# Optimization experiments

Hardware: AMD Instinct MI355X
Metric: run time of the kernel (lower is better)

## Reference

```python
import jax, jax.numpy as jnp
import numpy as np

B, D, S = 128, 256, 512
K, H, NCLS = 50, 256, 2
THRES = 0.3  # conceptshap threshold


def _l2norm(x, axis):
    n = jnp.sqrt(jnp.sum(x * x, axis=axis, keepdims=True))
    return x / jnp.maximum(n, 1e-12)


def setup_inputs() -> dict:
    key = jax.random.key(0)
    ks = jax.random.split(key, 6)
    return {
        "f_input": jax.random.normal(ks[0], (B, D, S), dtype=jnp.float32),
        "targets": jax.random.uniform(ks[1], (B,), dtype=jnp.float32),
        "topic_vector": jax.random.uniform(ks[2], (D, K), minval=-0.5, maxval=0.5, dtype=jnp.float32),
        "rec_vector_1": jax.random.uniform(ks[3], (K, H), minval=-0.5, maxval=0.5, dtype=jnp.float32),
        "rec_vector_2": jax.random.uniform(ks[4], (H, D), minval=-0.5, maxval=0.5, dtype=jnp.float32),
        "Wc": jax.random.normal(ks[5], (D, NCLS), dtype=jnp.float32) * 0.05,
        "bc": jnp.zeros((NCLS,), dtype=jnp.float32),
        "causal": 0,
    }


def reference(f_input, targets, topic_vector, rec_vector_1, rec_vector_2, Wc, bc, causal):
    # text path (n=3), model_name != 'transformer' -> swap to [B, S, D]
    x = jnp.swapaxes(f_input, 1, 2)                # [B, S, D]
    x_n = _l2norm(x, axis=-1)                      # F.normalize(dim=n-1)
    tv_n = _l2norm(topic_vector, axis=0)           # [D, K], column-normalized

    topic_prob = jnp.einsum('bsd,dk->bsk', x, tv_n)      # [B, S, K]
    topic_prob_n = jnp.einsum('bsd,dk->bsk', x_n, tv_n)  # [B, S, K]

    # conceptshap: no softmax, hard threshold mask
    mask = (topic_prob_n > THRES).astype(topic_prob.dtype)
    topic_prob_am = topic_prob * mask
    topic_prob_sum = jnp.sum(topic_prob_am, axis=-1, keepdims=True) + 0.001
    topic_prob_nn = topic_prob_am / (topic_prob_sum + 1e-8)

    rec_layer_1 = jax.nn.relu(jnp.einsum('bsk,kh->bsh', topic_prob_nn, rec_vector_1))
    rec_layer_2 = jnp.einsum('bsh,hd->bsd', rec_layer_1, rec_vector_2)  # [B, S, D]

    ae_loss = jnp.mean((x_n - rec_layer_2) ** 2)

    rec_out = jnp.swapaxes(rec_layer_2, 1, 2)      # back to [B, D, S]
    # frozen classifier: mean over seq + linear head
    pred = jnp.mean(rec_out, axis=-1) @ Wc + bc    # [B, NCLS]

    # concept_sim: mean of per-concept top-(B//4) similarity scores, negated
    res = topic_prob_n.reshape(-1, K).T            # [K, B*S]
    topv, _ = jax.lax.top_k(res, B // 4)
    concept_sim = -jnp.mean(topv)

    concept_far = jnp.mean(tv_n.T @ tv_n - jnp.eye(K, dtype=tv_n.dtype))

    return (pred, jnp.float32(0.0), concept_sim, concept_far, topic_prob_nn, ae_loss)
```

## Files before the change

kernel.cpp:

```cpp
#include <hip/hip_runtime.h>
#include <math.h>

#define BB 128
#define DD 256
#define SS 512
#define KK 50
#define HH 256
#define TS 64
#define NBLK (BB * SS / TS)
#define BS (BB * SS)

#define CHUNK 1024
#define NCH (BS / CHUNK)
#define NCHBLK (KK * NCH / 4)
#define TOPK 32
#define MAXSURV 512
#define NSUB (TS / 16)

#define TVN_OFF 0
#define TVNT_OFF (TVN_OFF + DD * KK)
#define TPNT_OFF (TVNT_OFF + KK * DD)
#define PREDACC_OFF (TPNT_OFF + KK * BS)
#define AE_OFF (PREDACC_OFF + BB * DD)
#define SIM_OFF (AE_OFF + 1)
#define CNT_OFF (AE_OFF + 2)
#define SIMD_OFF (AE_OFF + 3)
#define LIST_OFF (AE_OFF + 4)
#define CAND_OFF (LIST_OFF + MAXSURV)
#define NZERO (BB * DD + 4)

#define OUT_NN_OFF 259
#define OUT_AE_IDX (OUT_NN_OFF + KK * BS)

__device__ __forceinline__ unsigned fkey(float f) {
  unsigned u = __float_as_uint(f);
  return (u & 0x80000000u) ? ~u : (u | 0x80000000u);
}
__device__ __forceinline__ float keyval(unsigned T) {
  unsigned u = (T & 0x80000000u) ? (T & 0x7FFFFFFFu) : ~T;
  return __uint_as_float(u);
}

__global__ __launch_bounds__(256) void tvn_kernel(const float* __restrict__ tv,
                                                  float* __restrict__ tvn,
                                                  float* __restrict__ tvnT,
                                                  float* __restrict__ zbase) {
  __shared__ float red[256];
  const int k = blockIdx.x, t = threadIdx.x;
  {
    const int gid = k * 256 + t;
    for (int i = gid; i < NZERO; i += KK * 256) zbase[i] = 0.0f;
  }
  float v = tv[t * KK + k];
  red[t] = v * v;
  __syncthreads();
  for (int off = 128; off > 0; off >>= 1) {
    if (t < off) red[t] += red[t + off];
    __syncthreads();
  }
  float inv = 1.0f / fmaxf(sqrtf(red[0]), 1e-12f);
  const float nv = v * inv;
  tvn[t * KK + k] = nv;
  tvnT[k * DD + t] = nv;
}

__global__ __launch_bounds__(256, 4) void main_kernel(
    const float* __restrict__ f_input, const float* __restrict__ tvnT,
    float* __restrict__ out_nn, float* __restrict__ tpn_t,
    float* __restrict__ ae_acc, int* __restrict__ surv_cnt,
    int* __restrict__ surv_list) {
  __shared__ int wflag[4];

  const int blk = blockIdx.x;
  const int b = blk >> 3;
  const int s0 = (blk & 7) * TS;
  const int t = threadIdx.x;
  const int lane = t & 63;
  const int wid = t >> 6;
  const int kb = __builtin_amdgcn_readfirstlane(wid);

  const float* tvk[13];
  bool kval[13];
  #pragma unroll
  for (int j = 0; j < 13; ++j) {
    const int k = 4 * j + kb;
    kval[j] = (k < KK);
    tvk[j] = tvnT + (size_t)(kval[j] ? k : (KK - 1)) * DD;
  }

  const float* xp = f_input + (size_t)b * DD * SS + s0 + lane;

  float acc[13];
  #pragma unroll
  for (int j = 0; j < 13; ++j) acc[j] = 0.0f;

  float xb[2][4];
  #pragma unroll
  for (int i = 0; i < 4; ++i) xb[0][i] = xp[(size_t)i * SS];

  float s2 = 0.0f;
  int buf = 0;
  for (int part = 0; part < 8; ++part) {
    float p = 0.0f;
    #pragma unroll
    for (int dd = 0; dd < 32; dd += 4) {
      const int d0 = part * 32 + dd;
      const int dn = (d0 + 4 < DD) ? (d0 + 4) : 0;
      #pragma unroll
      for (int i = 0; i < 4; ++i) xb[buf ^ 1][i] = xp[(size_t)(dn + i) * SS];
      const float x0 = xb[buf][0], x1 = xb[buf][1], x2 = xb[buf][2], x3 = xb[buf][3];
      p += x0 * x0; p += x1 * x1; p += x2 * x2; p += x3 * x3;
      #pragma unroll
      for (int j = 0; j < 13; ++j) {
        const float4 tq = *(const float4*)(tvk[j] + d0);
        acc[j] += x0 * tq.x; acc[j] += x1 * tq.y;
        acc[j] += x2 * tq.z; acc[j] += x3 * tq.w;
      }
      buf ^= 1;
    }
    s2 = (part == 0) ? p : (s2 + p);
  }
  const float invn = 1.0f / fmaxf(sqrtf(s2), 1e-12f);

  bool m = false;
  const size_t gs = (size_t)b * SS + s0 + lane;
  #pragma unroll
  for (int j = 0; j < 13; ++j) {
    if (kval[j]) {
      const int k = 4 * j + kb;
      const float o = acc[j] * invn;
      tpn_t[(size_t)k * BS + gs] = o;
      m |= (o > 0.3f);
    }
  }

  const int w = __any((int)m);
  if (lane == 0) wflag[wid] = w;
  __syncthreads();
  const int any = wflag[0] | wflag[1] | wflag[2] | wflag[3];

  if (!any) {
    float* ob = out_nn + ((size_t)b * SS + s0) * KK;
    for (int p2 = t; p2 < TS * KK; p2 += 256) ob[p2] = 0.0f;
    if (t == 0) atomicAdd(ae_acc, (float)TS);
    return;
  }
  if (t == 0) {
    const int idx = atomicAdd(surv_cnt, 1);
    if (idx < MAXSURV) surv_list[idx] = blk;
  }
}

__global__ __launch_bounds__(256) void chunk_surv_kernel(
    const float* __restrict__ tpn_t, float* __restrict__ cand,
    const float* __restrict__ f_input, const float* __restrict__ rec1,
    const float* __restrict__ rec2, const int* __restrict__ surv_cnt,
    const int* __restrict__ surv_list, float* __restrict__ out_nn,
    float* __restrict__ predacc, float* __restrict__ ae_acc) {
  __shared__ __align__(16) float NNk[KK * 20];
  __shared__ __align__(16) float R1t[HH * 20];
  __shared__ float nprt[16][17];
  __shared__ float nrm[16], invn[16];
  __shared__ float pm[8 * DD];
  __shared__ float red4[4];

  const int t = threadIdx.x;
  const int lane = t & 63, wid = t >> 6;

  if (blockIdx.x < NCHBLK) {
    const int gchunk = blockIdx.x * 4 + wid;
    const int k = gchunk >> 6;
    const int c = gchunk & (NCH - 1);
    const float* row = tpn_t + (size_t)k * BS + c * CHUNK;

    float v[16];
    unsigned key[16];
    #pragma unroll
    for (int j = 0; j < 16; ++j) {
      v[j] = row[lane + j * 64];
      key[j] = fkey(v[j]);
    }
    unsigned T = 0;
    for (int bit = 31; bit >= 0; --bit) {
      const unsigned ct = T | (1u << bit);
      int cnt = 0;
      #pragma unroll
      for (int j = 0; j < 16; ++j) cnt += (key[j] >= ct) ? 1 : 0;
      #pragma unroll
      for (int off = 1; off < 64; off <<= 1) cnt += __shfl_xor(cnt, off);
      if (cnt >= TOPK) T = ct;
    }
    int cg = 0;
    #pragma unroll
    for (int j = 0; j < 16; ++j) cg += (key[j] > T) ? 1 : 0;
    int incl = cg;
    #pragma unroll
    for (int off = 1; off < 64; off <<= 1) {
      int y = __shfl_up(incl, off);
      if (lane >= off) incl += y;
    }
    const int excl = incl - cg;
    const int total_gt = __shfl(incl, 63);

    float* cb = cand + (size_t)gchunk * TOPK;
    int pos = excl;
    #pragma unroll
    for (int j = 0; j < 16; ++j) {
      if (key[j] > T) cb[pos++] = v[j];
    }
    if (lane < TOPK - total_gt) cb[total_gt + lane] = keyval(T);
    return;
  }

  const int bid = blockIdx.x - NCHBLK;
  int cnt = *surv_cnt;
  if (cnt > MAXSURV) cnt = MAXSURV;
  const int ntask = NSUB * cnt;

  for (int task = bid; task < ntask; task += 64) {
    const int blk = surv_list[task / NSUB];
    const int q = task % NSUB;
    const int b = blk >> 3;
    const int s0 = (blk & 7) * TS + q * 16;
    const float* fb = f_input + (size_t)b * DD * SS;
    const size_t gs0 = (size_t)b * SS + s0;

    for (int p = t; p < KK * 16; p += 256) {
      const int k = p >> 4, ss = p & 15;
      NNk[k * 20 + ss] = tpn_t[(size_t)k * BS + gs0 + ss];
    }
    {
      const int ss = t & 15, part = t >> 4;
      const float* xc = fb + (size_t)(part * 16) * SS + s0 + ss;
      float p = 0.0f;
      #pragma unroll
      for (int i = 0; i < 16; ++i) {
        const float v = xc[(size_t)i * SS];
        p += v * v;
      }
      nprt[part][ss] = p;
    }
    __syncthreads();
    if (t < 16) {
      float s2 = 0.0f;
      #pragma unroll
      for (int i = 0; i < 16; ++i) s2 += nprt[i][t];
      const float n = fmaxf(sqrtf(s2), 1e-12f);
      nrm[t] = n;
      invn[t] = 1.0f / n;
      float sm = 0.0f;
      for (int k = 0; k < KK; ++k) {
        const float tpn = NNk[k * 20 + t];
        sm += (tpn > 0.3f) ? tpn * n : 0.0f;
      }
      const float idv = 1.0f / (sm + 0.001f + 1e-8f);
      for (int k = 0; k < KK; ++k) {
        const float tpn = NNk[k * 20 + t];
        NNk[k * 20 + t] = (tpn > 0.3f) ? tpn * n * idv : 0.0f;
      }
    }
    __syncthreads();

    for (int p = t; p < 16 * KK; p += 256) {
      const int ss = p / KK, k = p - ss * KK;
      out_nn[(gs0 + ss) * KK + k] = NNk[k * 20 + ss];
    }

    {
      float a[16];
      #pragma unroll
      for (int i = 0; i < 16; ++i) a[i] = 0.0f;
      #pragma unroll 2
      for (int k = 0; k < KK; ++k) {
        const float r = rec1[k * HH + t];
        const float4* np = (const float4*)&NNk[k * 20];
        #pragma unroll
        for (int qq = 0; qq < 4; ++qq) {
          const float4 nv = np[qq];
          a[qq * 4 + 0] += nv.x * r;
          a[qq * 4 + 1] += nv.y * r;
          a[qq * 4 + 2] += nv.z * r;
          a[qq * 4 + 3] += nv.w * r;
        }
      }
      #pragma unroll
      for (int i = 0; i < 16; ++i) R1t[t * 20 + i] = fmaxf(a[i], 0.0f);
    }
    __syncthreads();

    const int tx = t & 31, ty = t >> 5;
    const int d0 = tx * 8, sb = ty * 2;
    float c2[2][8];
    #pragma unroll
    for (int i = 0; i < 2; ++i)
      #pragma unroll
      for (int j = 0; j < 8; ++j) c2[i][j] = 0.0f;
    for (int h0 = 0; h0 < HH; h0 += 8) {
      float4 B0[8], B1[8];
      #pragma unroll
      for (int u = 0; u < 8; ++u) {
        B0[u] = *(const float4*)(rec2 + (h0 + u) * DD + d0);
        B1[u] = *(const float4*)(rec2 + (h0 + u) * DD + d0 + 4);
      }
      #pragma unroll
      for (int u = 0; u < 8; ++u) {
        const float2 a01 = *(const float2*)(&R1t[(h0 + u) * 20 + sb]);
        const float bv[8] = {B0[u].x, B0[u].y, B0[u].z, B0[u].w,
                             B1[u].x, B1[u].y, B1[u].z, B1[u].w};
        #pragma unroll
        for (int j = 0; j < 8; ++j) {
          c2[0][j] += a01.x * bv[j];
          c2[1][j] += a01.y * bv[j];
        }
      }
    }
    #pragma unroll
    for (int j = 0; j < 8; ++j) pm[ty * DD + d0 + j] = c2[0][j] + c2[1][j];
    __syncthreads();
    {
      float sum = 0.0f;
      #pragma unroll
      for (int r = 0; r < 8; ++r) sum += pm[r * DD + t];
      atomicAdd(&predacc[(size_t)b * DD + t], sum);
    }
    float e = 0.0f;
    #pragma unroll
    for (int j = 0; j < 8; ++j) {
      #pragma unroll
      for (int i = 0; i < 2; ++i) {
        const float x = fb[(size_t)(d0 + j) * SS + s0 + sb + i];
        const float diff = x * invn[sb + i] - c2[i][j];
        e += diff * diff;
      }
    }
    #pragma unroll
    for (int off = 1; off < 64; off <<= 1) e += __shfl_xor(e, off);
    if (lane == 0) red4[wid] = e;
    __syncthreads();
    if (t == 0) atomicAdd(ae_acc, red4[0] + red4[1] + red4[2] + red4[3]);
    __syncthreads();
  }
}

__global__ __launch_bounds__(256) void merge_finalize_kernel(
    const float* __restrict__ cand, const float* __restrict__ predacc,
    const float* __restrict__ Wc, const float* __restrict__ bc,
    const float* __restrict__ ae_acc, float* __restrict__ sim_acc,
    unsigned* __restrict__ sim_done, const float* __restrict__ tvn,
    float* __restrict__ out) {
  __shared__ float r0[256], r1[256];
  const int blk = blockIdx.x;
  const int t = threadIdx.x;

  if (blk >= BB) {
    if (t < 64) {
      const int k = blk - BB;
      const int lane = t;
      const float* row = cand + (size_t)k * (NCH * TOPK);
      float v[32];
      unsigned key[32];
      #pragma unroll
      for (int j = 0; j < 32; ++j) {
        v[j] = row[lane + j * 64];
        key[j] = fkey(v[j]);
      }
      unsigned T = 0;
      for (int bit = 31; bit >= 0; --bit) {
        const unsigned ct = T | (1u << bit);
        int cnt = 0;
        #pragma unroll
        for (int j = 0; j < 32; ++j) cnt += (key[j] >= ct) ? 1 : 0;
        #pragma unroll
        for (int off = 1; off < 64; off <<= 1) cnt += __shfl_xor(cnt, off);
        if (cnt >= TOPK) T = ct;
      }
      float s = 0.0f;
      int cgt = 0;
      #pragma unroll
      for (int j = 0; j < 32; ++j) {
        if (key[j] > T) { s += v[j]; cgt++; }
      }
      #pragma unroll
      for (int off = 1; off < 64; off <<= 1) {
        s += __shfl_xor(s, off);
        cgt += __shfl_xor(cgt, off);
      }
      if (lane == 0) {
        atomicAdd(sim_acc, s + (float)(TOPK - cgt) * keyval(T));
        __threadfence();
        const unsigned c = atomicAdd(sim_done, 1u);
        if (c == KK - 1) {
          __threadfence();
          const float tot = atomicAdd(sim_acc, 0.0f);
          out[257] = -tot * (1.0f / (float)(KK * TOPK));
        }
      }
    }
    return;
  }

  const float s = predacc[(size_t)blk * DD + t];
  r0[t] = s * Wc[t * 2 + 0];
  r1[t] = s * Wc[t * 2 + 1];
  __syncthreads();
  for (int off = 128; off > 0; off >>= 1) {
    if (t < off) { r0[t] += r0[t + off]; r1[t] += r1[t + off]; }
    __syncthreads();
  }
  if (t == 0) {
    out[blk * 2 + 0] = r0[0] * (1.0f / (float)SS) + bc[0];
    out[blk * 2 + 1] = r1[0] * (1.0f / (float)SS) + bc[1];
    if (blk == 0) {
      out[256] = 0.0f;
      out[OUT_AE_IDX] = (*ae_acc) * (1.0f / ((float)BB * (float)SS * (float)DD));
    }
  }
  if (blk == 0) {
    __syncthreads();
    float rs = 0.0f;
    for (int k = 0; k < KK; ++k) rs += tvn[t * KK + k];
    r0[t] = rs * rs;
    __syncthreads();
    for (int off = 128; off > 0; off >>= 1) {
      if (t < off) r0[t] += r0[t + off];
      __syncthreads();
    }
    if (t == 0) out[258] = (r0[0] - (float)KK) / ((float)KK * (float)KK);
  }
}

extern "C" void kernel_launch(void* const* d_in, const int* in_sizes, int n_in,
                              void* d_out, int out_size, void* d_ws, size_t ws_size,
                              hipStream_t stream) {
  (void)in_sizes; (void)n_in; (void)out_size; (void)ws_size;
  const float* f_input = (const float*)d_in[0];
  const float* tv = (const float*)d_in[2];
  const float* rec1 = (const float*)d_in[3];
  const float* rec2 = (const float*)d_in[4];
  const float* Wc = (const float*)d_in[5];
  const float* bc = (const float*)d_in[6];

  float* out = (float*)d_out;
  float* ws = (float*)d_ws;
  float* tvn = ws + TVN_OFF;
  float* tvnT = ws + TVNT_OFF;
  float* tpn_t = ws + TPNT_OFF;
  float* predacc = ws + PREDACC_OFF;
  float* ae_acc = ws + AE_OFF;
  float* sim_acc = ws + SIM_OFF;
  int* surv_cnt = (int*)(ws + CNT_OFF);
  unsigned* sim_done = (unsigned*)(ws + SIMD_OFF);
  int* surv_list = (int*)(ws + LIST_OFF);
  float* cand = ws + CAND_OFF;

  tvn_kernel<<<KK, 256, 0, stream>>>(tv, tvn, tvnT, predacc);
  main_kernel<<<NBLK, 256, 0, stream>>>(f_input, tvnT, out + OUT_NN_OFF, tpn_t,
                                        ae_acc, surv_cnt, surv_list);
  chunk_surv_kernel<<<NCHBLK + 64, 256, 0, stream>>>(
      tpn_t, cand, f_input, rec1, rec2, surv_cnt, surv_list,
      out + OUT_NN_OFF, predacc, ae_acc);
  merge_finalize_kernel<<<BB + KK, 256, 0, stream>>>(
      cand, predacc, Wc, bc, ae_acc, sim_acc, sim_done, tvn, out);
}
```

Baseline: 231.0 us.

## Register-block two positions per thread and split concepts across block pairs

The projection kernel now uses 128-position tiles. Each thread loads two adjacent positions with float2 and accumulates both against every topic-vector load. Each tile's 50 concepts are split across two blocks, 8 waves with interleaved k, so per-thread accumulators stay small while topic-vector loads per FMA are halved. The all-zero decision is combined across the two blocks with a per-tile atomic flag and counter, and the block that finishes last records the survivor or the zero fill. The cost is that each input tile is now read by two blocks, plus some extra atomics and synchronisation.

```diff
diff --git a/kernel.cpp b/kernel.cpp
--- a/kernel.cpp
+++ b/kernel.cpp
@@ -6,8 +6,9 @@
 #define SS 512
 #define KK 50
 #define HH 256
-#define TS 64
-#define NBLK (BB * SS / TS)
+#define TS 128
+#define NTILES (BB * SS / TS)
+#define NBLK (NTILES * 2)
 #define BS (BB * SS)
 
 #define CHUNK 1024
@@ -25,9 +26,11 @@
 #define SIM_OFF (AE_OFF + 1)
 #define CNT_OFF (AE_OFF + 2)
 #define SIMD_OFF (AE_OFF + 3)
-#define LIST_OFF (AE_OFF + 4)
+#define TFLAG_OFF (AE_OFF + 4)
+#define TCNT_OFF (TFLAG_OFF + NTILES)
+#define NZERO (BB * DD + 4 + 2 * NTILES)
+#define LIST_OFF (TCNT_OFF + NTILES)
 #define CAND_OFF (LIST_OFF + MAXSURV)
-#define NZERO (BB * DD + 4)
 
 #define OUT_NN_OFF 259
 #define OUT_AE_IDX (OUT_NN_OFF + KK * BS)
@@ -68,86 +71,108 @@
     const float* __restrict__ f_input, const float* __restrict__ tvnT,
     float* __restrict__ out_nn, float* __restrict__ tpn_t,
     float* __restrict__ ae_acc, int* __restrict__ surv_cnt,
-    int* __restrict__ surv_list) {
+    int* __restrict__ surv_list, int* __restrict__ tile_flag,
+    int* __restrict__ tile_cnt) {
   __shared__ int wflag[4];
+  __shared__ int decision;
 
   const int blk = blockIdx.x;
-  const int b = blk >> 3;
-  const int s0 = (blk & 7) * TS;
+  const int tile = blk >> 1;
+  const int half = blk & 1;
+  const int b = tile >> 2;
+  const int s0 = (tile & 3) * TS;
   const int t = threadIdx.x;
   const int lane = t & 63;
   const int wid = t >> 6;
-  const int kb = __builtin_amdgcn_readfirstlane(wid);
-
-  const float* tvk[13];
-  bool kval[13];
+  const int kb = __builtin_amdgcn_readfirstlane(half * 4 + wid);
+
+  const float* tvk[7];
+  bool kval[7];
   #pragma unroll
-  for (int j = 0; j < 13; ++j) {
-    const int k = 4 * j + kb;
+  for (int j = 0; j < 7; ++j) {
+    const int k = kb + 8 * j;
     kval[j] = (k < KK);
     tvk[j] = tvnT + (size_t)(kval[j] ? k : (KK - 1)) * DD;
   }
 
-  const float* xp = f_input + (size_t)b * DD * SS + s0 + lane;
-
-  float acc[13];
+  const float* xp = f_input + (size_t)b * DD * SS + s0 + 2 * lane;
+
+  float acc0[7], acc1[7];
   #pragma unroll
-  for (int j = 0; j < 13; ++j) acc[j] = 0.0f;
-
-  float xb[2][4];
+  for (int j = 0; j < 7; ++j) { acc0[j] = 0.0f; acc1[j] = 0.0f; }
+
+  float2 xb[2][4];
   #pragma unroll
-  for (int i = 0; i < 4; ++i) xb[0][i] = xp[(size_t)i * SS];
-
-  float s2 = 0.0f;
+  for (int i = 0; i < 4; ++i) xb[0][i] = *(const float2*)(xp + (size_t)i * SS);
+
+  float s2_0 = 0.0f, s2_1 = 0.0f;
   int buf = 0;
   for (int part = 0; part < 8; ++part) {
-    float p = 0.0f;
+    float p0 = 0.0f, p1 = 0.0f;
     #pragma unroll
     for (int dd = 0; dd < 32; dd += 4) {
       const int d0 = part * 32 + dd;
       const int dn = (d0 + 4 < DD) ? (d0 + 4) : 0;
       #pragma unroll
-      for (int i = 0; i < 4; ++i) xb[buf ^ 1][i] = xp[(size_t)(dn + i) * SS];
-      const float x0 = xb[buf][0], x1 = xb[buf][1], x2 = xb[buf][2], x3 = xb[buf][3];
-      p += x0 * x0; p += x1 * x1; p += x2 * x2; p += x3 * x3;
-      #pragma unroll
-      for (int j = 0; j < 13; ++j) {
+      for (int i = 0; i < 4; ++i) xb[buf ^ 1][i] = *(const float2*)(xp + (size_t)(dn + i) * SS);
+      const float2 xa = xb[buf][0], xc2 = xb[buf][1], xc3 = xb[buf][2], xc4 = xb[buf][3];
+      p0 += xa.x * xa.x; p0 += xc2.x * xc2.x; p0 += xc3.x * xc3.x; p0 += xc4.x * xc4.x;
+      p1 += xa.y * xa.y; p1 += xc2.y * xc2.y; p1 += xc3.y * xc3.y; p1 += xc4.y * xc4.y;
+      #pragma unroll
+      for (int j = 0; j < 7; ++j) {
         const float4 tq = *(const float4*)(tvk[j] + d0);
-        acc[j] += x0 * tq.x; acc[j] += x1 * tq.y;
-        acc[j] += x2 * tq.z; acc[j] += x3 * tq.w;
+        acc0[j] += xa.x * tq.x; acc0[j] += xc2.x * tq.y;
+        acc0[j] += xc3.x * tq.z; acc0[j] += xc4.x * tq.w;
+        acc1[j] += xa.y * tq.x; acc1[j] += xc2.y * tq.y;
+        acc1[j] += xc3.y * tq.z; acc1[j] += xc4.y * tq.w;
       }
       buf ^= 1;
     }
-    s2 = (part == 0) ? p : (s2 + p);
-  }
-  const float invn = 1.0f / fmaxf(sqrtf(s2), 1e-12f);
+    s2_0 = (part == 0) ? p0 : (s2_0 + p0);
+    s2_1 = (part == 0) ? p1 : (s2_1 + p1);
+  }
+  const float i0 = 1.0f / fmaxf(sqrtf(s2_0), 1e-12f);
+  const float i1 = 1.0f / fmaxf(sqrtf(s2_1), 1e-12f);
 
   bool m = false;
-  const size_t gs = (size_t)b * SS + s0 + lane;
+  const size_t gs = (size_t)b * SS + s0 + 2 * lane;
   #pragma unroll
-  for (int j = 0; j < 13; ++j) {
+  for (int j = 0; j < 7; ++j) {
     if (kval[j]) {
-      const int k = 4 * j + kb;
-      const float o = acc[j] * invn;
-      tpn_t[(size_t)k * BS + gs] = o;
-      m |= (o > 0.3f);
+      const int k = kb + 8 * j;
+      float2 o;
+      o.x = acc0[j] * i0;
+      o.y = acc1[j] * i1;
+      *(float2*)(tpn_t + (size_t)k * BS + gs) = o;
+      m = m | (o.x > 0.3f) | (o.y > 0.3f);
     }
   }
 
   const int w = __any((int)m);
   if (lane == 0) wflag[wid] = w;
   __syncthreads();
-  const int any = wflag[0] | wflag[1] | wflag[2] | wflag[3];
-
-  if (!any) {
+  const int blockAny = wflag[0] | wflag[1] | wflag[2] | wflag[3];
+
+  if (t == 0) {
+    const int old = atomicOr(&tile_flag[tile], blockAny);
+    const int done = atomicAdd(&tile_cnt[tile], 1);
+    int dec = 0;
+    if (done == 1) {
+      const int fl = old | blockAny;
+      if (fl) {
+        const int idx = atomicAdd(surv_cnt, 1);
+        if (idx < MAXSURV) surv_list[idx] = tile;
+      } else {
+        atomicAdd(ae_acc, (float)TS);
+        dec = 1;
+      }
+    }
+    decision = dec;
+  }
+  __syncthreads();
+  if (decision) {
     float* ob = out_nn + ((size_t)b * SS + s0) * KK;
     for (int p2 = t; p2 < TS * KK; p2 += 256) ob[p2] = 0.0f;
-    if (t == 0) atomicAdd(ae_acc, (float)TS);
-    return;
-  }
-  if (t == 0) {
-    const int idx = atomicAdd(surv_cnt, 1);
-    if (idx < MAXSURV) surv_list[idx] = blk;
   }
 }
 
@@ -218,10 +243,10 @@
   const int ntask = NSUB * cnt;
 
   for (int task = bid; task < ntask; task += 64) {
-    const int blk = surv_list[task / NSUB];
+    const int tile = surv_list[task / NSUB];
     const int q = task % NSUB;
-    const int b = blk >> 3;
-    const int s0 = (blk & 7) * TS + q * 16;
+    const int b = tile >> 2;
+    const int s0 = (tile & 3) * TS + q * 16;
     const float* fb = f_input + (size_t)b * DD * SS;
     const size_t gs0 = (size_t)b * SS + s0;
 
@@ -450,12 +475,15 @@
   float* sim_acc = ws + SIM_OFF;
   int* surv_cnt = (int*)(ws + CNT_OFF);
   unsigned* sim_done = (unsigned*)(ws + SIMD_OFF);
+  int* tile_flag = (int*)(ws + TFLAG_OFF);
+  int* tile_cnt = (int*)(ws + TCNT_OFF);
   int* surv_list = (int*)(ws + LIST_OFF);
   float* cand = ws + CAND_OFF;
 
   tvn_kernel<<<KK, 256, 0, stream>>>(tv, tvn, tvnT, predacc);
   main_kernel<<<NBLK, 256, 0, stream>>>(f_input, tvnT, out + OUT_NN_OFF, tpn_t,
-                                        ae_acc, surv_cnt, surv_list);
+                                        ae_acc, surv_cnt, surv_list,
+                                        tile_flag, tile_cnt);
   chunk_surv_kernel<<<NCHBLK + 64, 256, 0, stream>>>(
       tpn_t, cand, f_input, rec1, rec2, surv_cnt, surv_list,
       out + OUT_NN_OFF, predacc, ae_acc);
```

Measured after the change: 226.4 us. 1.02x faster.

## Process two sequence positions per thread, prefetch rec weights, batch rec1 loads

Applied to the files above, without the earlier changes.

The main kernel tile grows from 64 to 128 positions, and each thread now computes two adjacent positions using float2 loads. This reuses each topic-vector load across twice the work and halves the block count. The surviving-tile path gets an early exit, a warm-up pass that reads rec1/rec2 into cache and writes their sum to a sink buffer, and rec1 loads batched ten at a time. The risks are higher register pressure in main_kernel (two accumulators per concept) and coarser survival granularity: one position above threshold now sends a whole 128-position tile through the slow path.

```diff
diff --git a/kernel.cpp b/kernel.cpp
--- a/kernel.cpp
+++ b/kernel.cpp
@@ -6,7 +6,7 @@
 #define SS 512
 #define KK 50
 #define HH 256
-#define TS 64
+#define TS 128
 #define NBLK (BB * SS / TS)
 #define BS (BB * SS)
 
@@ -25,9 +25,10 @@
 #define SIM_OFF (AE_OFF + 1)
 #define CNT_OFF (AE_OFF + 2)
 #define SIMD_OFF (AE_OFF + 3)
+#define NZERO (BB * DD + 4)
 #define LIST_OFF (AE_OFF + 4)
-#define CAND_OFF (LIST_OFF + MAXSURV)
-#define NZERO (BB * DD + 4)
+#define SINK_OFF (LIST_OFF + MAXSURV)
+#define CAND_OFF (SINK_OFF + 64 * 256)
 
 #define OUT_NN_OFF 259
 #define OUT_AE_IDX (OUT_NN_OFF + KK * BS)
@@ -72,8 +73,8 @@
   __shared__ int wflag[4];
 
   const int blk = blockIdx.x;
-  const int b = blk >> 3;
-  const int s0 = (blk & 7) * TS;
+  const int b = blk >> 2;
+  const int s0 = (blk & 3) * TS;
   const int t = threadIdx.x;
   const int lane = t & 63;
   const int wid = t >> 6;
@@ -88,49 +89,56 @@
     tvk[j] = tvnT + (size_t)(kval[j] ? k : (KK - 1)) * DD;
   }
 
-  const float* xp = f_input + (size_t)b * DD * SS + s0 + lane;
-
-  float acc[13];
+  const float* xp = f_input + (size_t)b * DD * SS + s0 + 2 * lane;
+
+  float acc0[13], acc1[13];
   #pragma unroll
-  for (int j = 0; j < 13; ++j) acc[j] = 0.0f;
-
-  float xb[2][4];
+  for (int j = 0; j < 13; ++j) { acc0[j] = 0.0f; acc1[j] = 0.0f; }
+
+  float2 xb[2][4];
   #pragma unroll
-  for (int i = 0; i < 4; ++i) xb[0][i] = xp[(size_t)i * SS];
-
-  float s2 = 0.0f;
+  for (int i = 0; i < 4; ++i) xb[0][i] = *(const float2*)(xp + (size_t)i * SS);
+
+  float s2_0 = 0.0f, s2_1 = 0.0f;
   int buf = 0;
   for (int part = 0; part < 8; ++part) {
-    float p = 0.0f;
+    float p0 = 0.0f, p1 = 0.0f;
     #pragma unroll
     for (int dd = 0; dd < 32; dd += 4) {
       const int d0 = part * 32 + dd;
       const int dn = (d0 + 4 < DD) ? (d0 + 4) : 0;
       #pragma unroll
-      for (int i = 0; i < 4; ++i) xb[buf ^ 1][i] = xp[(size_t)(dn + i) * SS];
-      const float x0 = xb[buf][0], x1 = xb[buf][1], x2 = xb[buf][2], x3 = xb[buf][3];
-      p += x0 * x0; p += x1 * x1; p += x2 * x2; p += x3 * x3;
+      for (int i = 0; i < 4; ++i) xb[buf ^ 1][i] = *(const float2*)(xp + (size_t)(dn + i) * SS);
+      const float2 xa = xb[buf][0], xc2 = xb[buf][1], xc3 = xb[buf][2], xc4 = xb[buf][3];
+      p0 += xa.x * xa.x; p0 += xc2.x * xc2.x; p0 += xc3.x * xc3.x; p0 += xc4.x * xc4.x;
+      p1 += xa.y * xa.y; p1 += xc2.y * xc2.y; p1 += xc3.y * xc3.y; p1 += xc4.y * xc4.y;
       #pragma unroll
       for (int j = 0; j < 13; ++j) {
         const float4 tq = *(const float4*)(tvk[j] + d0);
-        acc[j] += x0 * tq.x; acc[j] += x1 * tq.y;
-        acc[j] += x2 * tq.z; acc[j] += x3 * tq.w;
+        acc0[j] += xa.x * tq.x; acc0[j] += xc2.x * tq.y;
+        acc0[j] += xc3.x * tq.z; acc0[j] += xc4.x * tq.w;
+        acc1[j] += xa.y * tq.x; acc1[j] += xc2.y * tq.y;
+        acc1[j] += xc3.y * tq.z; acc1[j] += xc4.y * tq.w;
       }
       buf ^= 1;
     }
-    s2 = (part == 0) ? p : (s2 + p);
-  }
-  const float invn = 1.0f / fmaxf(sqrtf(s2), 1e-12f);
+    s2_0 = (part == 0) ? p0 : (s2_0 + p0);
+    s2_1 = (part == 0) ? p1 : (s2_1 + p1);
+  }
+  const float i0 = 1.0f / fmaxf(sqrtf(s2_0), 1e-12f);
+  const float i1 = 1.0f / fmaxf(sqrtf(s2_1), 1e-12f);
 
   bool m = false;
-  const size_t gs = (size_t)b * SS + s0 + lane;
+  const size_t gs = (size_t)b * SS + s0 + 2 * lane;
   #pragma unroll
   for (int j = 0; j < 13; ++j) {
     if (kval[j]) {
       const int k = 4 * j + kb;
-      const float o = acc[j] * invn;
-      tpn_t[(size_t)k * BS + gs] = o;
-      m |= (o > 0.3f);
+      float2 o;
+      o.x = acc0[j] * i0;
+      o.y = acc1[j] * i1;
+      *(float2*)(tpn_t + (size_t)k * BS + gs) = o;
+      m = m | (o.x > 0.3f) | (o.y > 0.3f);
     }
   }
 
@@ -156,7 +164,8 @@
     const float* __restrict__ f_input, const float* __restrict__ rec1,
     const float* __restrict__ rec2, const int* __restrict__ surv_cnt,
     const int* __restrict__ surv_list, float* __restrict__ out_nn,
-    float* __restrict__ predacc, float* __restrict__ ae_acc) {
+    float* __restrict__ predacc, float* __restrict__ ae_acc,
+    float* __restrict__ sink) {
   __shared__ __align__(16) float NNk[KK * 20];
   __shared__ __align__(16) float R1t[HH * 20];
   __shared__ float nprt[16][17];
@@ -216,12 +225,30 @@
   int cnt = *surv_cnt;
   if (cnt > MAXSURV) cnt = MAXSURV;
   const int ntask = NSUB * cnt;
+  if (bid >= ntask) return;
+
+  {
+    float wsum = 0.0f;
+    const float4* r1q = (const float4*)rec1;
+    const float4* r2q = (const float4*)rec2;
+    #pragma unroll 4
+    for (int i = t; i < KK * HH / 4; i += 256) {
+      const float4 v = r1q[i];
+      wsum += v.x + v.y + v.z + v.w;
+    }
+    #pragma unroll 8
+    for (int i = t; i < HH * DD / 4; i += 256) {
+      const float4 v = r2q[i];
+      wsum += v.x + v.y + v.z + v.w;
+    }
+    sink[bid * 256 + t] = wsum;
+  }
 
   for (int task = bid; task < ntask; task += 64) {
-    const int blk = surv_list[task / NSUB];
+    const int tile = surv_list[task / NSUB];
     const int q = task % NSUB;
-    const int b = blk >> 3;
-    const int s0 = (blk & 7) * TS + q * 16;
+    const int b = tile >> 2;
+    const int s0 = (tile & 3) * TS + q * 16;
     const float* fb = f_input + (size_t)b * DD * SS;
     const size_t gs0 = (size_t)b * SS + s0;
 
@@ -270,17 +297,22 @@
       float a[16];
       #pragma unroll
       for (int i = 0; i < 16; ++i) a[i] = 0.0f;
-      #pragma unroll 2
-      for (int k = 0; k < KK; ++k) {
-        const float r = rec1[k * HH + t];
-        const float4* np = (const float4*)&NNk[k * 20];
+      for (int k0 = 0; k0 < KK; k0 += 10) {
+        float rb[10];
         #pragma unroll
-        for (int qq = 0; qq < 4; ++qq) {
-          const float4 nv = np[qq];
-          a[qq * 4 + 0] += nv.x * r;
-          a[qq * 4 + 1] += nv.y * r;
-          a[qq * 4 + 2] += nv.z * r;
-          a[qq * 4 + 3] += nv.w * r;
+        for (int u = 0; u < 10; ++u) rb[u] = rec1[(k0 + u) * HH + t];
+        #pragma unroll
+        for (int u = 0; u < 10; ++u) {
+          const float r = rb[u];
+          const float4* np = (const float4*)&NNk[(k0 + u) * 20];
+          #pragma unroll
+          for (int qq = 0; qq < 4; ++qq) {
+            const float4 nv = np[qq];
+            a[qq * 4 + 0] += nv.x * r;
+            a[qq * 4 + 1] += nv.y * r;
+            a[qq * 4 + 2] += nv.z * r;
+            a[qq * 4 + 3] += nv.w * r;
+          }
         }
       }
       #pragma unroll
@@ -451,6 +483,7 @@
   int* surv_cnt = (int*)(ws + CNT_OFF);
   unsigned* sim_done = (unsigned*)(ws + SIMD_OFF);
   int* surv_list = (int*)(ws + LIST_OFF);
+  float* sink = ws + SINK_OFF;
   float* cand = ws + CAND_OFF;
 
   tvn_kernel<<<KK, 256, 0, stream>>>(tv, tvn, tvnT, predacc);
@@ -458,7 +491,7 @@
                                         ae_acc, surv_cnt, surv_list);
   chunk_surv_kernel<<<NCHBLK + 64, 256, 0, stream>>>(
       tpn_t, cand, f_input, rec1, rec2, surv_cnt, surv_list,
-      out + OUT_NN_OFF, predacc, ae_acc);
+      out + OUT_NN_OFF, predacc, ae_acc, sink);
   merge_finalize_kernel<<<BB + KK, 256, 0, stream>>>(
       cand, predacc, Wc, bc, ae_acc, sim_acc, sim_done, tvn, out);
 }
```

New measurement: 239.4 us. 1.04x slower.
